# Kernel optimization log

Hardware: AMD Instinct MI355X
Metric: run time of the kernel (lower is better)

## Reference

```python
import jax, jax.numpy as jnp
import numpy as np

B, L, C, D = 4, 2048, 64, 4


def setup_inputs() -> dict:
    key = jax.random.key(0)
    k1, k2, k3, k4 = jax.random.split(key, 4)
    # |A| kept < ~0.92 so the length-2048 recurrence stays bounded
    A_re = jax.random.uniform(k1, (B, L, C, D), jnp.float32, -0.65, 0.65)
    A_im = jax.random.uniform(k2, (B, L, C, D), jnp.float32, -0.65, 0.65)
    X_re = jax.random.normal(k3, (B, L, C, D, D), jnp.float32)
    X_im = jax.random.normal(k4, (B, L, C, D, D), jnp.float32)
    return {"A_re": A_re, "A_im": A_im, "X_re": X_re, "X_im": X_im}


def _combine(c1, c2):
    # first-order linear recurrence combine: (a, x) o (b, y) = (b*a, b*x + y)
    a1, x1 = c1
    a2, x2 = c2
    return a2 * a1, a2 * x1 + x2


def reference(A_re, A_im, X_re, X_im):
    # Diagonal complex pscan: Y[t] = A[t] * Y[t-1] + X[t], elementwise,
    # with diagonal A [B,L,C,D] broadcast over the trailing D dim of X [B,L,C,D,D]
    A = (A_re + 1j * A_im).astype(jnp.complex64)[..., None]  # [B,L,C,D,1]
    X = (X_re + 1j * X_im).astype(jnp.complex64)             # [B,L,C,D,D]
    _, Y = jax.lax.associative_scan(_combine, (A, X), axis=1)
    # return real view [B,L,C,D,D,2] (real, imag) like torch.view_as_real
    return jnp.stack([Y.real, Y.imag], axis=-1)
```

## Files before the change

### kernel.cpp

```cpp
#include <hip/hip_runtime.h>

#define BB 4
#define LL 2048
#define CC 64
#define DD 4
#define NN (CC * DD * DD)
#define AN (CC * DD)
#define GG 256
#define TT (LL / GG)
#define SEGLEN 16
#define NSEG (GG / SEGLEN)

typedef float f32x4 __attribute__((ext_vector_type(4)));


__global__ __launch_bounds__(256) void pscan_phase1(
    const float* __restrict__ A_re, const float* __restrict__ A_im,
    const f32x4* __restrict__ X_re4, const f32x4* __restrict__ X_im4,
    f32x4* __restrict__ agg) {
  int u  = blockIdx.x * 256 + threadIdx.x;
  int n4 = u & (AN - 1);
  int bg = u >> 8;
  int g  = bg & (GG - 1);
  int b  = bg >> 8;
  int t0 = g * TT;
  int baseA = (b * LL + t0) * AN + n4;
  int baseX = (b * LL + t0) * AN + n4;

  float p_re = 1.f, p_im = 0.f;
  float s_re[4] = {0.f, 0.f, 0.f, 0.f};
  float s_im[4] = {0.f, 0.f, 0.f, 0.f};

#pragma unroll
  for (int t = 0; t < TT; ++t) {
    float are = A_re[baseA + t * AN];
    float aim = A_im[baseA + t * AN];
    f32x4 xr  = X_re4[baseX + t * AN];
    f32x4 xi  = X_im4[baseX + t * AN];
    float npre = are * p_re - aim * p_im;
    float npim = are * p_im + aim * p_re;
    p_re = npre; p_im = npim;
#pragma unroll
    for (int j = 0; j < 4; ++j) {
      float nsre = are * s_re[j] - aim * s_im[j] + xr[j];
      float nsim = are * s_im[j] + aim * s_re[j] + xi[j];
      s_re[j] = nsre; s_im[j] = nsim;
    }
  }
  int ab = (b * GG + g) * NN + n4 * 4;
#pragma unroll
  for (int j = 0; j < 4; ++j) {
    f32x4 v = {p_re, p_im, s_re[j], s_im[j]};
    agg[ab + j] = v;
  }
}

__global__ __launch_bounds__(256) void pscan_phase2a(
    f32x4* __restrict__ agg, f32x4* __restrict__ segAgg) {
  int u   = blockIdx.x * 256 + threadIdx.x;
  int n   = u & (NN - 1);
  int r   = u >> 10;
  int seg = r & (NSEG - 1);
  int b   = r >> 4;
  int base = (b * GG + seg * SEGLEN) * NN + n;

  f32x4 v[SEGLEN];
#pragma unroll
  for (int t = 0; t < SEGLEN; ++t) v[t] = agg[base + t * NN];

  float rp_re = 1.f, rp_im = 0.f, rs_re = 0.f, rs_im = 0.f;
#pragma unroll
  for (int t = 0; t < SEGLEN; ++t) {
    f32x4 cur = v[t];
    f32x4 run = {rp_re, rp_im, rs_re, rs_im};
    agg[base + t * NN] = run;
    float np_re = cur.x * rp_re - cur.y * rp_im;
    float np_im = cur.x * rp_im + cur.y * rp_re;
    float ns_re = cur.x * rs_re - cur.y * rs_im + cur.z;
    float ns_im = cur.x * rs_im + cur.y * rs_re + cur.w;
    rp_re = np_re; rp_im = np_im; rs_re = ns_re; rs_im = ns_im;
  }
  f32x4 tot = {rp_re, rp_im, rs_re, rs_im};
  segAgg[(b * NSEG + seg) * NN + n] = tot;
}

__global__ __launch_bounds__(256) void pscan_phase2b(f32x4* __restrict__ segAgg) {
  int u = blockIdx.x * 256 + threadIdx.x;
  int n = u & (NN - 1);
  int b = u >> 10;
  int base = b * NSEG * NN + n;

  f32x4 v[NSEG];
#pragma unroll
  for (int s = 0; s < NSEG; ++s) v[s] = segAgg[base + s * NN];

  float rp_re = 1.f, rp_im = 0.f, rs_re = 0.f, rs_im = 0.f;
#pragma unroll
  for (int s = 0; s < NSEG; ++s) {
    f32x4 cur = v[s];
    f32x4 run = {rp_re, rp_im, rs_re, rs_im};
    segAgg[base + s * NN] = run;
    float np_re = cur.x * rp_re - cur.y * rp_im;
    float np_im = cur.x * rp_im + cur.y * rp_re;
    float ns_re = cur.x * rs_re - cur.y * rs_im + cur.z;
    float ns_im = cur.x * rs_im + cur.y * rs_re + cur.w;
    rp_re = np_re; rp_im = np_im; rs_re = ns_re; rs_im = ns_im;
  }
}

__global__ __launch_bounds__(256) void pscan_phase3(
    const float* __restrict__ A_re, const float* __restrict__ A_im,
    const f32x4* __restrict__ X_re4, const f32x4* __restrict__ X_im4,
    const f32x4* __restrict__ agg, const f32x4* __restrict__ segAgg,
    f32x4* __restrict__ out4) {
  int u  = blockIdx.x * 256 + threadIdx.x;
  int n4 = u & (AN - 1);
  int bg = u >> 8;
  int g  = bg & (GG - 1);
  int b  = bg >> 8;
  int t0 = g * TT;
  int seg = g >> 4;
  int baseA = (b * LL + t0) * AN + n4;
  int baseX = (b * LL + t0) * AN + n4;
  int ab = (b * GG + g) * NN + n4 * 4;
  int sb = (b * NSEG + seg) * NN + n4 * 4;

  float y_re[4], y_im[4];
#pragma unroll
  for (int j = 0; j < 4; ++j) {
    f32x4 la = agg[ab + j];
    f32x4 sa = segAgg[sb + j];
    y_re[j] = la.x * sa.z - la.y * sa.w + la.z;
    y_im[j] = la.x * sa.w + la.y * sa.z + la.w;
  }

  int ob = (b * LL + t0) * (2 * AN) + n4 * 2;
#pragma unroll
  for (int t = 0; t < TT; ++t) {
    float are = A_re[baseA + t * AN];
    float aim = A_im[baseA + t * AN];
    f32x4 xr  = X_re4[baseX + t * AN];
    f32x4 xi  = X_im4[baseX + t * AN];
#pragma unroll
    for (int j = 0; j < 4; ++j) {
      float ny_re = are * y_re[j] - aim * y_im[j] + xr[j];
      float ny_im = are * y_im[j] + aim * y_re[j] + xi[j];
      y_re[j] = ny_re; y_im[j] = ny_im;
    }
    f32x4 o0 = {y_re[0], y_im[0], y_re[1], y_im[1]};
    f32x4 o1 = {y_re[2], y_im[2], y_re[3], y_im[3]};
    out4[ob + t * (2 * AN)]     = o0;
    out4[ob + t * (2 * AN) + 1] = o1;
  }
}

extern "C" void kernel_launch(void* const* d_in, const int* in_sizes, int n_in,
                              void* d_out, int out_size, void* d_ws, size_t ws_size,
                              hipStream_t stream) {
  const float* A_re = (const float*)d_in[0];
  const float* A_im = (const float*)d_in[1];
  const f32x4* X_re4 = (const f32x4*)d_in[2];
  const f32x4* X_im4 = (const f32x4*)d_in[3];
  f32x4* out4 = (f32x4*)d_out;

  f32x4* agg    = (f32x4*)d_ws;
  f32x4* segAgg = (f32x4*)((char*)d_ws + (size_t)BB * GG * NN * 16);

  const int total = BB * GG * AN;
  pscan_phase1<<<total / 256, 256, 0, stream>>>(A_re, A_im, X_re4, X_im4, agg);
  pscan_phase2a<<<(BB * NSEG * NN) / 256, 256, 0, stream>>>(agg, segAgg);
  pscan_phase2b<<<(BB * NN) / 256, 256, 0, stream>>>(segAgg);
  pscan_phase3<<<total / 256, 256, 0, stream>>>(A_re, A_im, X_re4, X_im4, agg, segAgg, out4);
}
```

Baseline: 156.1 us.

## Fuse scan phases into one cooperative kernel with register-cached inputs

Adds a single cooperative kernel that runs all four pscan phases separated by grid-wide syncs, keeping the A and X tiles in registers so phase 3 does not re-read them from global memory. This removes three kernel launch gaps and a second pass over the inputs. In exchange it needs 1024 blocks to be co-resident (the launch bounds ask for 4 blocks per CU), holds many live registers across the syncs, and leaves most threads idle during the two serial middle phases. It falls back to the original four-kernel path if a cooperative launch is not possible.

```diff
diff --git a/kernel.cpp b/kernel.cpp
--- a/kernel.cpp
+++ b/kernel.cpp
@@ -1,4 +1,7 @@
 #include <hip/hip_runtime.h>
+#include <hip/hip_cooperative_groups.h>
+
+namespace cg = cooperative_groups;
 
 #define BB 4
 #define LL 2048
@@ -13,6 +16,130 @@
 
 typedef float f32x4 __attribute__((ext_vector_type(4)));
 
+__global__ __launch_bounds__(256, 4) void pscan_fused(
+    const float* __restrict__ A_re, const float* __restrict__ A_im,
+    const f32x4* __restrict__ X_re4, const f32x4* __restrict__ X_im4,
+    f32x4* __restrict__ agg, f32x4* __restrict__ segAgg,
+    f32x4* __restrict__ out4) {
+  cg::grid_group grid = cg::this_grid();
+
+  int u  = blockIdx.x * 256 + threadIdx.x;
+  int n4 = u & (AN - 1);
+  int bg = u >> 8;
+  int g  = bg & (GG - 1);
+  int b  = bg >> 8;
+  int t0 = g * TT;
+  int base = (b * LL + t0) * AN + n4;
+
+  float ar[TT], ai[TT];
+  f32x4 xr[TT], xi[TT];
+#pragma unroll
+  for (int t = 0; t < TT; ++t) {
+    ar[t] = A_re[base + t * AN];
+    ai[t] = A_im[base + t * AN];
+    xr[t] = X_re4[base + t * AN];
+    xi[t] = X_im4[base + t * AN];
+  }
+
+  float p_re = 1.f, p_im = 0.f;
+  float s_re[4] = {0.f, 0.f, 0.f, 0.f};
+  float s_im[4] = {0.f, 0.f, 0.f, 0.f};
+#pragma unroll
+  for (int t = 0; t < TT; ++t) {
+    float are = ar[t], aim = ai[t];
+    float npre = are * p_re - aim * p_im;
+    float npim = are * p_im + aim * p_re;
+    p_re = npre; p_im = npim;
+#pragma unroll
+    for (int j = 0; j < 4; ++j) {
+      float nsre = are * s_re[j] - aim * s_im[j] + xr[t][j];
+      float nsim = are * s_im[j] + aim * s_re[j] + xi[t][j];
+      s_re[j] = nsre; s_im[j] = nsim;
+    }
+  }
+  int ab = (b * GG + g) * NN + n4 * 4;
+#pragma unroll
+  for (int j = 0; j < 4; ++j) {
+    f32x4 v = {p_re, p_im, s_re[j], s_im[j]};
+    agg[ab + j] = v;
+  }
+
+  __threadfence();
+  grid.sync();
+  __threadfence();
+
+  if (u < BB * NSEG * NN) {
+    int n   = u & (NN - 1);
+    int r   = u >> 10;
+    int seg = r & (NSEG - 1);
+    int b2  = r >> 4;
+    int base2 = (b2 * GG + seg * SEGLEN) * NN + n;
+    float rp_re = 1.f, rp_im = 0.f, rs_re = 0.f, rs_im = 0.f;
+    for (int t = 0; t < SEGLEN; ++t) {
+      f32x4 cur = agg[base2 + t * NN];
+      f32x4 run = {rp_re, rp_im, rs_re, rs_im};
+      agg[base2 + t * NN] = run;
+      float np_re = cur.x * rp_re - cur.y * rp_im;
+      float np_im = cur.x * rp_im + cur.y * rp_re;
+      float ns_re = cur.x * rs_re - cur.y * rs_im + cur.z;
+      float ns_im = cur.x * rs_im + cur.y * rs_re + cur.w;
+      rp_re = np_re; rp_im = np_im; rs_re = ns_re; rs_im = ns_im;
+    }
+    f32x4 tot = {rp_re, rp_im, rs_re, rs_im};
+    segAgg[(b2 * NSEG + seg) * NN + n] = tot;
+  }
+
+  __threadfence();
+  grid.sync();
+  __threadfence();
+
+  if (u < BB * NN) {
+    int n  = u & (NN - 1);
+    int b3 = u >> 10;
+    int base3 = b3 * NSEG * NN + n;
+    float rp_re = 1.f, rp_im = 0.f, rs_re = 0.f, rs_im = 0.f;
+    for (int s = 0; s < NSEG; ++s) {
+      f32x4 cur = segAgg[base3 + s * NN];
+      f32x4 run = {rp_re, rp_im, rs_re, rs_im};
+      segAgg[base3 + s * NN] = run;
+      float np_re = cur.x * rp_re - cur.y * rp_im;
+      float np_im = cur.x * rp_im + cur.y * rp_re;
+      float ns_re = cur.x * rs_re - cur.y * rs_im + cur.z;
+      float ns_im = cur.x * rs_im + cur.y * rs_re + cur.w;
+      rp_re = np_re; rp_im = np_im; rs_re = ns_re; rs_im = ns_im;
+    }
+  }
+
+  __threadfence();
+  grid.sync();
+  __threadfence();
+
+  int sb = (b * NSEG + (g >> 4)) * NN + n4 * 4;
+  float y_re[4], y_im[4];
+#pragma unroll
+  for (int j = 0; j < 4; ++j) {
+    f32x4 la = agg[ab + j];
+    f32x4 sa = segAgg[sb + j];
+    y_re[j] = la.x * sa.z - la.y * sa.w + la.z;
+    y_im[j] = la.x * sa.w + la.y * sa.z + la.w;
+  }
+
+  int ob = (b * LL + t0) * (2 * AN) + n4 * 2;
+#pragma unroll
+  for (int t = 0; t < TT; ++t) {
+    float are = ar[t], aim = ai[t];
+#pragma unroll
+    for (int j = 0; j < 4; ++j) {
+      float ny_re = are * y_re[j] - aim * y_im[j] + xr[t][j];
+      float ny_im = are * y_im[j] + aim * y_re[j] + xi[t][j];
+      y_re[j] = ny_re; y_im[j] = ny_im;
+    }
+    f32x4 o0 = {y_re[0], y_im[0], y_re[1], y_im[1]};
+    f32x4 o1 = {y_re[2], y_im[2], y_re[3], y_im[3]};
+    out4[ob + t * (2 * AN)]     = o0;
+    out4[ob + t * (2 * AN) + 1] = o1;
+  }
+}
 
 __global__ __launch_bounds__(256) void pscan_phase1(
     const float* __restrict__ A_re, const float* __restrict__ A_im,
@@ -24,26 +151,24 @@
   int g  = bg & (GG - 1);
   int b  = bg >> 8;
   int t0 = g * TT;
-  int baseA = (b * LL + t0) * AN + n4;
-  int baseX = (b * LL + t0) * AN + n4;
+  int base = (b * LL + t0) * AN + n4;
 
   float p_re = 1.f, p_im = 0.f;
   float s_re[4] = {0.f, 0.f, 0.f, 0.f};
   float s_im[4] = {0.f, 0.f, 0.f, 0.f};
-
-#pragma unroll
-  for (int t = 0; t < TT; ++t) {
-    float are = A_re[baseA + t * AN];
-    float aim = A_im[baseA + t * AN];
-    f32x4 xr  = X_re4[baseX + t * AN];
-    f32x4 xi  = X_im4[baseX + t * AN];
+#pragma unroll
+  for (int t = 0; t < TT; ++t) {
+    float are = A_re[base + t * AN];
+    float aim = A_im[base + t * AN];
+    f32x4 xrv = X_re4[base + t * AN];
+    f32x4 xiv = X_im4[base + t * AN];
     float npre = are * p_re - aim * p_im;
     float npim = are * p_im + aim * p_re;
     p_re = npre; p_im = npim;
 #pragma unroll
     for (int j = 0; j < 4; ++j) {
-      float nsre = are * s_re[j] - aim * s_im[j] + xr[j];
-      float nsim = are * s_im[j] + aim * s_re[j] + xi[j];
+      float nsre = are * s_re[j] - aim * s_im[j] + xrv[j];
+      float nsim = are * s_im[j] + aim * s_re[j] + xiv[j];
       s_re[j] = nsre; s_im[j] = nsim;
     }
   }
@@ -63,15 +188,9 @@
   int seg = r & (NSEG - 1);
   int b   = r >> 4;
   int base = (b * GG + seg * SEGLEN) * NN + n;
-
-  f32x4 v[SEGLEN];
-#pragma unroll
-  for (int t = 0; t < SEGLEN; ++t) v[t] = agg[base + t * NN];
-
   float rp_re = 1.f, rp_im = 0.f, rs_re = 0.f, rs_im = 0.f;
-#pragma unroll
   for (int t = 0; t < SEGLEN; ++t) {
-    f32x4 cur = v[t];
+    f32x4 cur = agg[base + t * NN];
     f32x4 run = {rp_re, rp_im, rs_re, rs_im};
     agg[base + t * NN] = run;
     float np_re = cur.x * rp_re - cur.y * rp_im;
@@ -89,15 +208,9 @@
   int n = u & (NN - 1);
   int b = u >> 10;
   int base = b * NSEG * NN + n;
-
-  f32x4 v[NSEG];
-#pragma unroll
-  for (int s = 0; s < NSEG; ++s) v[s] = segAgg[base + s * NN];
-
   float rp_re = 1.f, rp_im = 0.f, rs_re = 0.f, rs_im = 0.f;
-#pragma unroll
   for (int s = 0; s < NSEG; ++s) {
-    f32x4 cur = v[s];
+    f32x4 cur = segAgg[base + s * NN];
     f32x4 run = {rp_re, rp_im, rs_re, rs_im};
     segAgg[base + s * NN] = run;
     float np_re = cur.x * rp_re - cur.y * rp_im;
@@ -119,11 +232,9 @@
   int g  = bg & (GG - 1);
   int b  = bg >> 8;
   int t0 = g * TT;
-  int seg = g >> 4;
-  int baseA = (b * LL + t0) * AN + n4;
-  int baseX = (b * LL + t0) * AN + n4;
+  int base = (b * LL + t0) * AN + n4;
   int ab = (b * GG + g) * NN + n4 * 4;
-  int sb = (b * NSEG + seg) * NN + n4 * 4;
+  int sb = (b * NSEG + (g >> 4)) * NN + n4 * 4;
 
   float y_re[4], y_im[4];
 #pragma unroll
@@ -133,18 +244,17 @@
     y_re[j] = la.x * sa.z - la.y * sa.w + la.z;
     y_im[j] = la.x * sa.w + la.y * sa.z + la.w;
   }
-
   int ob = (b * LL + t0) * (2 * AN) + n4 * 2;
 #pragma unroll
   for (int t = 0; t < TT; ++t) {
-    float are = A_re[baseA + t * AN];
-    float aim = A_im[baseA + t * AN];
-    f32x4 xr  = X_re4[baseX + t * AN];
-    f32x4 xi  = X_im4[baseX + t * AN];
+    float are = A_re[base + t * AN];
+    float aim = A_im[base + t * AN];
+    f32x4 xrv = X_re4[base + t * AN];
+    f32x4 xiv = X_im4[base + t * AN];
 #pragma unroll
     for (int j = 0; j < 4; ++j) {
-      float ny_re = are * y_re[j] - aim * y_im[j] + xr[j];
-      float ny_im = are * y_im[j] + aim * y_re[j] + xi[j];
+      float ny_re = are * y_re[j] - aim * y_im[j] + xrv[j];
+      float ny_im = are * y_im[j] + aim * y_re[j] + xiv[j];
       y_re[j] = ny_re; y_im[j] = ny_im;
     }
     f32x4 o0 = {y_re[0], y_im[0], y_re[1], y_im[1]};
@@ -166,9 +276,30 @@
   f32x4* agg    = (f32x4*)d_ws;
   f32x4* segAgg = (f32x4*)((char*)d_ws + (size_t)BB * GG * NN * 16);
 
-  const int total = BB * GG * AN;
-  pscan_phase1<<<total / 256, 256, 0, stream>>>(A_re, A_im, X_re4, X_im4, agg);
+  const int total  = BB * GG * AN;
+  const int blocks = total / 256;
+
+  static int coop_ok = -1;
+  if (coop_ok < 0) {
+    int dev = 0, ncu = 0, coop = 0, maxb = 0;
+    hipGetDevice(&dev);
+    hipDeviceGetAttribute(&ncu, hipDeviceAttributeMultiprocessorCount, dev);
+    hipDeviceGetAttribute(&coop, hipDeviceAttributeCooperativeLaunch, dev);
+    hipOccupancyMaxActiveBlocksPerMultiprocessor(&maxb, pscan_fused, 256, 0);
+    coop_ok = (coop && ncu > 0 && maxb * ncu >= blocks) ? 1 : 0;
+  }
+
+  if (coop_ok) {
+    void* args[] = {(void*)&A_re, (void*)&A_im, (void*)&X_re4, (void*)&X_im4,
+                    (void*)&agg, (void*)&segAgg, (void*)&out4};
+    hipError_t e = hipLaunchCooperativeKernel(pscan_fused, dim3(blocks), dim3(256),
+                                              args, 0, stream);
+    if (e == hipSuccess) return;
+    coop_ok = 0;
+  }
+
+  pscan_phase1<<<blocks, 256, 0, stream>>>(A_re, A_im, X_re4, X_im4, agg);
   pscan_phase2a<<<(BB * NSEG * NN) / 256, 256, 0, stream>>>(agg, segAgg);
   pscan_phase2b<<<(BB * NN) / 256, 256, 0, stream>>>(segAgg);
-  pscan_phase3<<<total / 256, 256, 0, stream>>>(A_re, A_im, X_re4, X_im4, agg, segAgg, out4);
-}
+  pscan_phase3<<<blocks, 256, 0, stream>>>(A_re, A_im, X_re4, X_im4, agg, segAgg, out4);
+}
```

Result: no change. 155.5 us (-0.4%).

## Fuse four-phase scan into one kernel with block-level LDS scan over time

Applied to the files above, without the earlier changes.

Replaces the three-level chunked scan (local aggregates, two carry passes, fixup) with a single kernel. Each block owns one (batch, channel-row) column, and each thread holds eight timesteps in registers. Carries come from a Hillis-Steele scan in shared memory. This removes the second read of the inputs, the workspace traffic and three launches. In exchange, adjacent threads now access addresses 4 KB apart, losing coalescing. The block swizzle also scatters neighbouring columns across XCDs.

```diff
diff --git a/kernel.cpp b/kernel.cpp
--- a/kernel.cpp
+++ b/kernel.cpp
@@ -6,145 +6,102 @@
 #define DD 4
 #define NN (CC * DD * DD)
 #define AN (CC * DD)
-#define GG 256
-#define TT (LL / GG)
-#define SEGLEN 16
-#define NSEG (GG / SEGLEN)
+#define TPB 256
+#define TT (LL / TPB)
 
 typedef float f32x4 __attribute__((ext_vector_type(4)));
 
-
-__global__ __launch_bounds__(256) void pscan_phase1(
+__global__ __launch_bounds__(256) void pscan_onepass(
     const float* __restrict__ A_re, const float* __restrict__ A_im,
     const f32x4* __restrict__ X_re4, const f32x4* __restrict__ X_im4,
-    f32x4* __restrict__ agg) {
-  int u  = blockIdx.x * 256 + threadIdx.x;
-  int n4 = u & (AN - 1);
-  int bg = u >> 8;
-  int g  = bg & (GG - 1);
-  int b  = bg >> 8;
-  int t0 = g * TT;
-  int baseA = (b * LL + t0) * AN + n4;
-  int baseX = (b * LL + t0) * AN + n4;
+    f32x4* __restrict__ out4) {
+  const int sid = (blockIdx.x & 7) * 128 + (blockIdx.x >> 3);
+  const int n4  = sid & (AN - 1);
+  const int b   = sid >> 8;
+  const int tid = threadIdx.x;
+  const int t0  = tid * TT;
+  const int base = (b * LL + t0) * AN + n4;
+
+  float ar[TT], ai[TT];
+  f32x4 xr[TT], xi[TT];
+#pragma unroll
+  for (int t = 0; t < TT; ++t) {
+    ar[t] = A_re[base + t * AN];
+    ai[t] = A_im[base + t * AN];
+    xr[t] = X_re4[base + t * AN];
+    xi[t] = X_im4[base + t * AN];
+  }
 
   float p_re = 1.f, p_im = 0.f;
   float s_re[4] = {0.f, 0.f, 0.f, 0.f};
   float s_im[4] = {0.f, 0.f, 0.f, 0.f};
-
 #pragma unroll
   for (int t = 0; t < TT; ++t) {
-    float are = A_re[baseA + t * AN];
-    float aim = A_im[baseA + t * AN];
-    f32x4 xr  = X_re4[baseX + t * AN];
-    f32x4 xi  = X_im4[baseX + t * AN];
-    float npre = are * p_re - aim * p_im;
-    float npim = are * p_im + aim * p_re;
+    const float are = ar[t], aim = ai[t];
+    const float npre = are * p_re - aim * p_im;
+    const float npim = are * p_im + aim * p_re;
     p_re = npre; p_im = npim;
 #pragma unroll
     for (int j = 0; j < 4; ++j) {
-      float nsre = are * s_re[j] - aim * s_im[j] + xr[j];
-      float nsim = are * s_im[j] + aim * s_re[j] + xi[j];
+      const float nsre = are * s_re[j] - aim * s_im[j] + xr[t][j];
+      const float nsim = are * s_im[j] + aim * s_re[j] + xi[t][j];
       s_re[j] = nsre; s_im[j] = nsim;
     }
   }
-  int ab = (b * GG + g) * NN + n4 * 4;
+
+  __shared__ float lds[TPB][11];
+  lds[tid][0] = p_re; lds[tid][1] = p_im;
 #pragma unroll
-  for (int j = 0; j < 4; ++j) {
-    f32x4 v = {p_re, p_im, s_re[j], s_im[j]};
-    agg[ab + j] = v;
+  for (int j = 0; j < 4; ++j) { lds[tid][2 + j] = s_re[j]; lds[tid][6 + j] = s_im[j]; }
+
+  float vp_re = p_re, vp_im = p_im;
+  float vs_re[4], vs_im[4];
+#pragma unroll
+  for (int j = 0; j < 4; ++j) { vs_re[j] = s_re[j]; vs_im[j] = s_im[j]; }
+
+  for (int d = 1; d < TPB; d <<= 1) {
+    __syncthreads();
+    float wp_re = 1.f, wp_im = 0.f;
+    float ws_re[4] = {0.f, 0.f, 0.f, 0.f};
+    float ws_im[4] = {0.f, 0.f, 0.f, 0.f};
+    if (tid >= d) {
+      wp_re = lds[tid - d][0]; wp_im = lds[tid - d][1];
+#pragma unroll
+      for (int j = 0; j < 4; ++j) { ws_re[j] = lds[tid - d][2 + j]; ws_im[j] = lds[tid - d][6 + j]; }
+    }
+    __syncthreads();
+    if (tid >= d) {
+      const float np_re = vp_re * wp_re - vp_im * wp_im;
+      const float np_im = vp_re * wp_im + vp_im * wp_re;
+#pragma unroll
+      for (int j = 0; j < 4; ++j) {
+        const float ns_re = vp_re * ws_re[j] - vp_im * ws_im[j] + vs_re[j];
+        const float ns_im = vp_re * ws_im[j] + vp_im * ws_re[j] + vs_im[j];
+        vs_re[j] = ns_re; vs_im[j] = ns_im;
+      }
+      vp_re = np_re; vp_im = np_im;
+      lds[tid][0] = vp_re; lds[tid][1] = vp_im;
+#pragma unroll
+      for (int j = 0; j < 4; ++j) { lds[tid][2 + j] = vs_re[j]; lds[tid][6 + j] = vs_im[j]; }
+    }
   }
-}
+  __syncthreads();
 
-__global__ __launch_bounds__(256) void pscan_phase2a(
-    f32x4* __restrict__ agg, f32x4* __restrict__ segAgg) {
-  int u   = blockIdx.x * 256 + threadIdx.x;
-  int n   = u & (NN - 1);
-  int r   = u >> 10;
-  int seg = r & (NSEG - 1);
-  int b   = r >> 4;
-  int base = (b * GG + seg * SEGLEN) * NN + n;
-
-  f32x4 v[SEGLEN];
+  float y_re[4] = {0.f, 0.f, 0.f, 0.f};
+  float y_im[4] = {0.f, 0.f, 0.f, 0.f};
+  if (tid > 0) {
 #pragma unroll
-  for (int t = 0; t < SEGLEN; ++t) v[t] = agg[base + t * NN];
-
-  float rp_re = 1.f, rp_im = 0.f, rs_re = 0.f, rs_im = 0.f;
-#pragma unroll
-  for (int t = 0; t < SEGLEN; ++t) {
-    f32x4 cur = v[t];
-    f32x4 run = {rp_re, rp_im, rs_re, rs_im};
-    agg[base + t * NN] = run;
-    float np_re = cur.x * rp_re - cur.y * rp_im;
-    float np_im = cur.x * rp_im + cur.y * rp_re;
-    float ns_re = cur.x * rs_re - cur.y * rs_im + cur.z;
-    float ns_im = cur.x * rs_im + cur.y * rs_re + cur.w;
-    rp_re = np_re; rp_im = np_im; rs_re = ns_re; rs_im = ns_im;
-  }
-  f32x4 tot = {rp_re, rp_im, rs_re, rs_im};
-  segAgg[(b * NSEG + seg) * NN + n] = tot;
-}
-
-__global__ __launch_bounds__(256) void pscan_phase2b(f32x4* __restrict__ segAgg) {
-  int u = blockIdx.x * 256 + threadIdx.x;
-  int n = u & (NN - 1);
-  int b = u >> 10;
-  int base = b * NSEG * NN + n;
-
-  f32x4 v[NSEG];
-#pragma unroll
-  for (int s = 0; s < NSEG; ++s) v[s] = segAgg[base + s * NN];
-
-  float rp_re = 1.f, rp_im = 0.f, rs_re = 0.f, rs_im = 0.f;
-#pragma unroll
-  for (int s = 0; s < NSEG; ++s) {
-    f32x4 cur = v[s];
-    f32x4 run = {rp_re, rp_im, rs_re, rs_im};
-    segAgg[base + s * NN] = run;
-    float np_re = cur.x * rp_re - cur.y * rp_im;
-    float np_im = cur.x * rp_im + cur.y * rp_re;
-    float ns_re = cur.x * rs_re - cur.y * rs_im + cur.z;
-    float ns_im = cur.x * rs_im + cur.y * rs_re + cur.w;
-    rp_re = np_re; rp_im = np_im; rs_re = ns_re; rs_im = ns_im;
-  }
-}
-
-__global__ __launch_bounds__(256) void pscan_phase3(
-    const float* __restrict__ A_re, const float* __restrict__ A_im,
-    const f32x4* __restrict__ X_re4, const f32x4* __restrict__ X_im4,
-    const f32x4* __restrict__ agg, const f32x4* __restrict__ segAgg,
-    f32x4* __restrict__ out4) {
-  int u  = blockIdx.x * 256 + threadIdx.x;
-  int n4 = u & (AN - 1);
-  int bg = u >> 8;
-  int g  = bg & (GG - 1);
-  int b  = bg >> 8;
-  int t0 = g * TT;
-  int seg = g >> 4;
-  int baseA = (b * LL + t0) * AN + n4;
-  int baseX = (b * LL + t0) * AN + n4;
-  int ab = (b * GG + g) * NN + n4 * 4;
-  int sb = (b * NSEG + seg) * NN + n4 * 4;
-
-  float y_re[4], y_im[4];
-#pragma unroll
-  for (int j = 0; j < 4; ++j) {
-    f32x4 la = agg[ab + j];
-    f32x4 sa = segAgg[sb + j];
-    y_re[j] = la.x * sa.z - la.y * sa.w + la.z;
-    y_im[j] = la.x * sa.w + la.y * sa.z + la.w;
+    for (int j = 0; j < 4; ++j) { y_re[j] = lds[tid - 1][2 + j]; y_im[j] = lds[tid - 1][6 + j]; }
   }
 
-  int ob = (b * LL + t0) * (2 * AN) + n4 * 2;
+  const int ob = (b * LL + t0) * (2 * AN) + n4 * 2;
 #pragma unroll
   for (int t = 0; t < TT; ++t) {
-    float are = A_re[baseA + t * AN];
-    float aim = A_im[baseA + t * AN];
-    f32x4 xr  = X_re4[baseX + t * AN];
-    f32x4 xi  = X_im4[baseX + t * AN];
+    const float are = ar[t], aim = ai[t];
 #pragma unroll
     for (int j = 0; j < 4; ++j) {
-      float ny_re = are * y_re[j] - aim * y_im[j] + xr[j];
-      float ny_im = are * y_im[j] + aim * y_re[j] + xi[j];
+      const float ny_re = are * y_re[j] - aim * y_im[j] + xr[t][j];
+      const float ny_im = are * y_im[j] + aim * y_re[j] + xi[t][j];
       y_re[j] = ny_re; y_im[j] = ny_im;
     }
     f32x4 o0 = {y_re[0], y_im[0], y_re[1], y_im[1]};
@@ -157,18 +114,13 @@
 extern "C" void kernel_launch(void* const* d_in, const int* in_sizes, int n_in,
                               void* d_out, int out_size, void* d_ws, size_t ws_size,
                               hipStream_t stream) {
-  const float* A_re = (const float*)d_in[0];
-  const float* A_im = (const float*)d_in[1];
+  const float* A_re  = (const float*)d_in[0];
+  const float* A_im  = (const float*)d_in[1];
   const f32x4* X_re4 = (const f32x4*)d_in[2];
   const f32x4* X_im4 = (const f32x4*)d_in[3];
   f32x4* out4 = (f32x4*)d_out;
+  (void)d_ws; (void)ws_size;
 
-  f32x4* agg    = (f32x4*)d_ws;
-  f32x4* segAgg = (f32x4*)((char*)d_ws + (size_t)BB * GG * NN * 16);
-
-  const int total = BB * GG * AN;
-  pscan_phase1<<<total / 256, 256, 0, stream>>>(A_re, A_im, X_re4, X_im4, agg);
-  pscan_phase2a<<<(BB * NSEG * NN) / 256, 256, 0, stream>>>(agg, segAgg);
-  pscan_phase2b<<<(BB * NN) / 256, 256, 0, stream>>>(segAgg);
-  pscan_phase3<<<total / 256, 256, 0, stream>>>(A_re, A_im, X_re4, X_im4, agg, segAgg, out4);
+  const int blocks = BB * AN;
+  pscan_onepass<<<blocks, TPB, 0, stream>>>(A_re, A_im, X_re4, X_im4, out4);
 }
```

After: 173.1 us. 10.9% more time.
